# Performance work log

Hardware: AMD Instinct MI355X
Metric: run time of the kernel (lower is better)

## Reference

```python
import jax, jax.numpy as jnp
import numpy as np

N = 50000      # nodes
E = 600000     # edges (before self loops)
F_IN = 128     # num_features
HID = 64       # num_hidden (per-head out channels of conv1)
HEADS = 8
NCLS = 16      # num_classes
NC = 16        # n_components (k_ricci feature dim)
NCP = 16       # n_components_p (e_poinc feature dim)


def _glorot(key, shape):
    lim = float(np.sqrt(6.0 / (shape[0] + shape[1])))
    return jax.random.uniform(key, shape, jnp.float32, -lim, lim)


def setup_inputs() -> dict:
    key = jax.random.key(0)
    ks = jax.random.split(key, 16)
    H1 = HEADS * HID  # 512
    return {
        "x": jax.random.normal(ks[0], (N, F_IN), jnp.float32),
        "edge_index": jax.random.randint(ks[1], (2, E), 0, N, jnp.int32),
        "alpha": jnp.ones((), jnp.float32),  # alpha_hp scalar
        "k_ricci": jax.random.normal(ks[2], (E + N, NC), jnp.float32),
        "e_poinc": jax.random.normal(ks[3], (N, NCP), jnp.float32),
        # conv1 params
        "W_src1": _glorot(ks[4], (F_IN, H1)),
        "h1_w1": _glorot(ks[5], (NC, HID)),
        "h1_w2": _glorot(ks[6], (HID, HID)),
        "h1_b2": jnp.zeros((HID,), jnp.float32),
        "p1_w1": _glorot(ks[7], (NCP, H1)),
        "p1_w2": _glorot(ks[8], (H1, H1)),
        "p1_b2": jnp.zeros((H1,), jnp.float32),
        "bias1": jnp.zeros((H1,), jnp.float32),
        # conv2 params (heads=1, concat=False)
        "W_src2": _glorot(ks[9], (H1, NCLS)),
        "h2_w1": _glorot(ks[10], (NC, NCLS)),
        "h2_w2": _glorot(ks[11], (NCLS, NCLS)),
        "h2_b2": jnp.zeros((NCLS,), jnp.float32),
        "p2_w1": _glorot(ks[12], (NCP, NCLS)),
        "p2_w2": _glorot(ks[13], (NCLS, NCLS)),
        "p2_b2": jnp.zeros((NCLS,), jnp.float32),
        "bias2": jnp.zeros((NCLS,), jnp.float32),
    }


def _segment_softmax(logits, seg, n):
    # PyG-style softmax over variable-sized segments, per channel.
    m = jax.ops.segment_max(logits, seg, num_segments=n)
    e = jnp.exp(logits - m[seg])
    s = jax.ops.segment_sum(e, seg, num_segments=n)
    return e / (s[seg] + 1e-16)


def _gat_layer(x, src, dst, k_ricci, e_poinc, alpha_hp,
               W_src, hw1, hw2, hb2, pw1, pw2, pb2, bias, H, C, concat):
    n = x.shape[0]
    xh = (x @ W_src).reshape(n, H, C)                                   # [N,H,C]
    # hmpnn MLP on per-edge Ricci features, then segment-softmax over SOURCE node
    edge_w = jax.nn.leaky_relu(k_ricci @ hw1, 0.2) @ hw2 + hb2          # [E',C]
    a = _segment_softmax(edge_w, src, n)                                # [E',C]
    msg = a[:, None, :] * xh[src]                                       # [E',H,C]
    agg = jax.ops.segment_sum(msg, dst, num_segments=n)                 # [N,H,C]
    out = agg.reshape(n, H * C) if concat else agg.mean(axis=1)
    out = out + bias
    # ham MLP on per-node Poincare features (+ extra leaky_relu, slope 0.01)
    p = jax.nn.leaky_relu(jax.nn.leaky_relu(e_poinc @ pw1, 0.2) @ pw2 + pb2, 0.01)
    return out + alpha_hp * p


def reference(x, edge_index, alpha, k_ricci, e_poinc,
              W_src1, h1_w1, h1_w2, h1_b2, p1_w1, p1_w2, p1_b2, bias1,
              W_src2, h2_w1, h2_w2, h2_b2, p2_w1, p2_w2, p2_b2, bias2):
    n = x.shape[0]
    loops = jnp.arange(n, dtype=edge_index.dtype)
    src = jnp.concatenate([edge_index[0], loops])   # add_self_loops
    dst = jnp.concatenate([edge_index[1], loops])
    h = _gat_layer(x, src, dst, k_ricci, e_poinc, alpha,
                   W_src1, h1_w1, h1_w2, h1_b2, p1_w1, p1_w2, p1_b2, bias1,
                   HEADS, HID, True)
    h = jax.nn.relu(h)
    o = _gat_layer(h, src, dst, k_ricci, e_poinc, alpha,
                   W_src2, h2_w1, h2_w2, h2_b2, p2_w1, p2_w2, p2_b2, bias2,
                   1, NCLS, False)
    return jax.nn.log_softmax(o, axis=1)
```

## Files before the change

kernel.cpp:

```cpp
#include <hip/hip_runtime.h>
#include <math.h>

#define N_NODES 50000
#define M_PAD   50048
#define N_EDGES 600000
#define E_TOT   650000
#define F_IN    128
#define HID     64
#define HEADS   8
#define H1      512
#define NCLS    16
#define NC      16
#define NCP     16
#define NBLK    ((N_NODES + 255) / 256)

typedef unsigned short u16;
typedef unsigned char  u8;
typedef __attribute__((ext_vector_type(8))) short short8;
typedef __attribute__((ext_vector_type(4))) float f32x4;
typedef __attribute__((ext_vector_type(2))) float f32x2;

__device__ __forceinline__ float bf2f(u16 h) {
    return __uint_as_float(((unsigned)h) << 16);
}
__device__ __forceinline__ u16 f2bf(float f) {
    unsigned u = __float_as_uint(f);
    u += 0x7fffu + ((u >> 16) & 1u);
    return (u16)(u >> 16);
}
__device__ __forceinline__ int edge_src(const int* __restrict__ ei, int e) {
    return (e < N_EDGES) ? ei[e] : (e - N_EDGES);
}
__device__ __forceinline__ int edge_dst(const int* __restrict__ ei, int e) {
    return (e < N_EDGES) ? ei[N_EDGES + e] : (e - N_EDGES);
}

__global__ __launch_bounds__(256) void count_k(const int* __restrict__ ei,
                                               int* __restrict__ src_cnt, int* __restrict__ dst_cnt) {
    int e = blockIdx.x * 256 + threadIdx.x;
    if (e >= E_TOT) return;
    atomicAdd(&src_cnt[edge_src(ei, e)], 1);
    atomicAdd(&dst_cnt[edge_dst(ei, e)], 1);
}

__global__ __launch_bounds__(256) void scanA_k(const int* __restrict__ src_cnt,
                                               const int* __restrict__ dst_cnt,
                                               int* __restrict__ partials) {
    int pass = blockIdx.x >= NBLK;
    int b = blockIdx.x - pass * NBLK;
    const int* cnt = pass ? dst_cnt : src_cnt;
    int idx = b * 256 + threadIdx.x;
    int v = (idx < N_NODES) ? cnt[idx] : 0;
    __shared__ int red[4];
    #pragma unroll
    for (int off = 32; off; off >>= 1) v += __shfl_down(v, off, 64);
    if ((threadIdx.x & 63) == 0) red[threadIdx.x >> 6] = v;
    __syncthreads();
    if (threadIdx.x == 0) partials[blockIdx.x] = red[0] + red[1] + red[2] + red[3];
}

__global__ __launch_bounds__(512) void scanB_k(int* __restrict__ partials) {
    __shared__ int lds[512];
    int t = threadIdx.x;
    int seg = t >> 8, i = t & 255;
    int v = (i < NBLK) ? partials[seg * NBLK + i] : 0;
    lds[t] = v;
    __syncthreads();
    for (int d = 1; d < 256; d <<= 1) {
        int x = (i >= d) ? lds[seg * 256 + i - d] : 0;
        __syncthreads();
        lds[t] += x;
        __syncthreads();
    }
    if (i < NBLK) partials[seg * NBLK + i] = lds[t] - v;
}

__global__ __launch_bounds__(256) void scanC_k(const int* __restrict__ src_cnt,
                                               const int* __restrict__ dst_cnt,
                                               const int* __restrict__ partials,
                                               int* __restrict__ src_off, int* __restrict__ dst_off) {
    int pass = blockIdx.x >= NBLK;
    int b = blockIdx.x - pass * NBLK;
    const int* cnt = pass ? dst_cnt : src_cnt;
    int* off = pass ? dst_off : src_off;
    int base = partials[blockIdx.x];
    __shared__ int lds[256];
    int t = threadIdx.x;
    int idx = b * 256 + t;
    int v = (idx < N_NODES) ? cnt[idx] : 0;
    lds[t] = v;
    __syncthreads();
    for (int d = 1; d < 256; d <<= 1) {
        int x = (t >= d) ? lds[t - d] : 0;
        __syncthreads();
        lds[t] += x;
        __syncthreads();
    }
    if (idx < N_NODES) off[idx] = base + lds[t] - v;
    if (b == 0 && t == 0) off[N_NODES] = E_TOT;
}

__global__ __launch_bounds__(256) void fill_csr_k(const int* __restrict__ ei,
                                                  const int* __restrict__ src_off, const int* __restrict__ dst_off,
                                                  int* __restrict__ src_cur, int* __restrict__ dst_cur,
                                                  int* __restrict__ src_list, int* __restrict__ rkd,
                                                  int* __restrict__ dsrc) {
    int e = blockIdx.x * 256 + threadIdx.x;
    if (e >= E_TOT) return;
    int s = edge_src(ei, e), d = edge_dst(ei, e);
    int pd = atomicAdd(&dst_cur[d], 1);
    int rd = dst_off[d] + pd;
    rkd[e] = rd;
    dsrc[rd] = s;
    int ps = atomicAdd(&src_cur[s], 1);
    src_list[src_off[s] + ps] = rd;
}

__global__ __launch_bounds__(256) void conv_a_k(const float* __restrict__ A, u16* __restrict__ Ap,
                                                int M, int Mp, int K) {
    int i = blockIdx.x * 256 + threadIdx.x;
    int total = (K >> 3) * Mp;
    if (i >= total) return;
    int r = i % Mp;
    int kb = i / Mp;
    u16* o = Ap + (size_t)i * 8;
    u16 tmp[8];
    if (r < M) {
        const float* a = A + (size_t)r * K + kb * 8;
        #pragma unroll
        for (int j = 0; j < 8; ++j) tmp[j] = f2bf(a[j]);
    } else {
        #pragma unroll
        for (int j = 0; j < 8; ++j) tmp[j] = 0;
    }
    *(ushort4*)o = *(ushort4*)tmp;
    *(ushort4*)(o + 4) = *(ushort4*)(tmp + 4);
}

__global__ __launch_bounds__(256) void conv_b_k(const float* __restrict__ B, u16* __restrict__ Bp,
                                                int K, int N) {
    int i = blockIdx.x * 256 + threadIdx.x;
    int total = (K >> 3) * N;
    if (i >= total) return;
    int n = i % N;
    int kb = i / N;
    u16 tmp[8];
    #pragma unroll
    for (int j = 0; j < 8; ++j) tmp[j] = f2bf(B[(size_t)(kb * 8 + j) * N + n]);
    u16* o = Bp + (size_t)i * 8;
    *(ushort4*)o = *(ushort4*)tmp;
    *(ushort4*)(o + 4) = *(ushort4*)(tmp + 4);
}

__device__ __forceinline__ void wfrag_one(const float* W, u16* o, int i, int K, int N) {
    int j = i & 7, lane = (i >> 3) & 63, rest = i >> 9;
    int nt = rest % (N / 16), ks = rest / (N / 16);
    int lm = lane & 15, quad = lane >> 4;
    int k = ks * 32 + quad * 8 + j, n = nt * 16 + lm;
    o[i] = (k < K) ? f2bf(W[(size_t)k * N + n]) : (u16)0;
}
__global__ __launch_bounds__(256) void wfrag_all_k(
    const float* __restrict__ h1w1, const float* __restrict__ h1w2,
    const float* __restrict__ h2w1, const float* __restrict__ h2w2,
    u16* __restrict__ w1f, u16* __restrict__ w2f,
    u16* __restrict__ w3f, u16* __restrict__ w4f) {
    int i = blockIdx.x * 256 + threadIdx.x;
    if (i < 2048)      wfrag_one(h1w1, w1f, i, 16, 64);
    else if (i < 6144) wfrag_one(h1w2, w2f, i - 2048, 64, 64);
    else if (i < 6656) wfrag_one(h2w1, w3f, i - 6144, 16, 16);
    else if (i < 7168) wfrag_one(h2w2, w4f, i - 6656, 16, 16);
}

template<int EPI>
__global__ __launch_bounds__(256) void mfma_gemm_k(
    const u16* __restrict__ Ap, const u16* __restrict__ Bp, u16* __restrict__ C,
    int M, int Mp, int Nn, int K,
    const float* __restrict__ bias, const u16* __restrict__ extra,
    const float* __restrict__ bias2, const float* __restrict__ alpha_p)
{
    const int t = threadIdx.x;
    const int wave = t >> 6, lane = t & 63;
    const int wm = (wave >> 1) * 64, wn = (wave & 1) * 64;
    const int bm = blockIdx.y * 128, bn = blockIdx.x * 128;
    const int lm = lane & 15, quad = lane >> 4;

    size_t rbase[4], cbase[4];
    #pragma unroll
    for (int mi = 0; mi < 4; ++mi) rbase[mi] = (size_t)(bm + wm + mi * 16 + lm) * 8;
    #pragma unroll
    for (int nj = 0; nj < 4; ++nj) cbase[nj] = (size_t)(bn + wn + nj * 16 + lm) * 8;

    f32x4 acc[4][4] = {};

    for (int k0 = 0; k0 < K; k0 += 32) {
        int kb = (k0 >> 3) + quad;
        size_t abase = (size_t)kb * Mp * 8;
        size_t bbase = (size_t)kb * Nn * 8;
        short8 af[4], bf_[4];
        #pragma unroll
        for (int mi = 0; mi < 4; ++mi) af[mi] = *(const short8*)(Ap + abase + rbase[mi]);
        #pragma unroll
        for (int nj = 0; nj < 4; ++nj) bf_[nj] = *(const short8*)(Bp + bbase + cbase[nj]);
        #pragma unroll
        for (int mi = 0; mi < 4; ++mi)
            #pragma unroll
            for (int nj = 0; nj < 4; ++nj)
                acc[mi][nj] = __builtin_amdgcn_mfma_f32_16x16x32_bf16(af[mi], bf_[nj], acc[mi][nj], 0, 0, 0);
    }

    const int orow = bm + wm + quad * 4;
    const int ocol = bn + wn + lm;
    if (EPI == 0) {
        #pragma unroll
        for (int mi = 0; mi < 4; ++mi)
            #pragma unroll
            for (int r = 0; r < 4; ++r) {
                int rr = orow + mi * 16 + r;
                if (rr >= M) continue;
                #pragma unroll
                for (int nj = 0; nj < 4; ++nj)
                    C[(size_t)rr * Nn + ocol + nj * 16] = f2bf(acc[mi][nj][r]);
            }
    } else {
        float alpha = *alpha_p;
        #pragma unroll
        for (int mi = 0; mi < 4; ++mi)
            #pragma unroll
            for (int r = 0; r < 4; ++r) {
                int rr = orow + mi * 16 + r;
                if (rr >= M) continue;
                #pragma unroll
                for (int nj = 0; nj < 4; ++nj) {
                    int c = ocol + nj * 16;
                    float v = acc[mi][nj][r] + bias[c];
                    v = v > 0.f ? v : 0.01f * v;
                    float o = bf2f(extra[(size_t)rr * Nn + c]) + bias2[c] + alpha * v;
                    o = fmaxf(o, 0.f);
                    C[(size_t)rr * Nn + c] = f2bf(o);
                }
            }
    }
}

__global__ __launch_bounds__(256) void gemm_t1_k(
    const float* __restrict__ ep, const float* __restrict__ W, u16* __restrict__ t1p)
{
    __shared__ float Bs[16][64];
    const int bm = blockIdx.y * 64, bn = blockIdx.x * 64;
    const int t = threadIdx.x;
    const int tx = t & 15, ty = t >> 4;
    *(float4*)&Bs[t >> 4][(t & 15) * 4] = *(const float4*)&W[(size_t)(t >> 4) * H1 + bn + (t & 15) * 4];
    __syncthreads();
    const int r0 = bm + ty * 4;
    const int c0 = bn + tx * 4;
    for (int i = 0; i < 4; ++i) {
        int r = r0 + i;
        if (r >= N_NODES) continue;
        float av[16];
        #pragma unroll
        for (int j4 = 0; j4 < 16; j4 += 4) {
            float4 v = *(const float4*)(ep + (size_t)r * NCP + j4);
            av[j4] = v.x; av[j4 + 1] = v.y; av[j4 + 2] = v.z; av[j4 + 3] = v.w;
        }
        u16 pk[4];
        #pragma unroll
        for (int q = 0; q < 4; ++q) {
            float s = 0.f;
            #pragma unroll
            for (int k = 0; k < 16; ++k) s = fmaf(av[k], Bs[k][tx * 4 + q], s);
            s = s > 0.f ? s : 0.2f * s;
            pk[q] = f2bf(s);
        }
        u16* o = t1p + ((size_t)(c0 >> 3) * M_PAD + r) * 8 + (c0 & 7);
        *(ushort4*)o = *(ushort4*)pk;
    }
}

__global__ __launch_bounds__(256) void gemm_n16_k(
    const u16* __restrict__ A, const float* __restrict__ B, float* __restrict__ C,
    int M, int K)
{
    __shared__ float As[16][64];
    __shared__ float Bs[64][16];
    const int row0 = blockIdx.x * 16;
    const int t = threadIdx.x;
    const int r = t >> 4, c = t & 15;
    const int ar = t >> 4, ak4 = (t & 15) * 4;
    const int bk = t >> 2, bc4 = (t & 3) * 4;
    float acc = 0.f;
    for (int k0 = 0; k0 < K; k0 += 64) {
        float4 av = make_float4(0.f, 0.f, 0.f, 0.f);
        if (row0 + ar < M) {
            ushort4 h4 = *(const ushort4*)(A + (size_t)(row0 + ar) * K + k0 + ak4);
            av = make_float4(bf2f(h4.x), bf2f(h4.y), bf2f(h4.z), bf2f(h4.w));
        }
        *(float4*)&As[ar][ak4] = av;
        *(float4*)&Bs[bk][bc4] = *(const float4*)(B + (size_t)(k0 + bk) * 16 + bc4);
        __syncthreads();
        #pragma unroll
        for (int kk = 0; kk < 64; ++kk)
            acc = fmaf(As[r][kk], Bs[kk][c], acc);
        __syncthreads();
    }
    if (row0 + r < M) C[(size_t)(row0 + r) * 16 + c] = acc;
}

#define TSTR 72
__global__ __launch_bounds__(256) void edge_mlps_k(
    const float* __restrict__ kr, const int* __restrict__ rkd,
    const u16* __restrict__ w1f, const u16* __restrict__ w2f, const float* __restrict__ b2a,
    const u16* __restrict__ w3f, const u16* __restrict__ w4f, const float* __restrict__ b2b,
    u16* __restrict__ ebd, u16* __restrict__ ebd2)
{
    __shared__ __align__(16) u16 T[4][16 * TSTR];
    const int t = threadIdx.x, wv = t >> 6, lane = t & 63;
    const int lm = lane & 15, quad = lane >> 4;
    const int tile = blockIdx.x * 4 + wv;
    const int e0 = tile * 16;
    if (e0 >= E_TOT) return;
    u16* Tw = T[wv];

    short8 W1[4], W2[2][4];
    #pragma unroll
    for (int nt = 0; nt < 4; ++nt) W1[nt] = *(const short8*)(w1f + ((size_t)nt * 64 + lane) * 8);
    #pragma unroll
    for (int ks = 0; ks < 2; ++ks)
        #pragma unroll
        for (int nt = 0; nt < 4; ++nt)
            W2[ks][nt] = *(const short8*)(w2f + (((size_t)ks * 4 + nt) * 64 + lane) * 8);
    short8 W3 = *(const short8*)(w3f + (size_t)lane * 8);
    short8 W4 = *(const short8*)(w4f + (size_t)lane * 8);
    float b2av[4];
    #pragma unroll
    for (int nt = 0; nt < 4; ++nt) b2av[nt] = b2a[nt * 16 + lm];
    float b2bv = b2b[lm];

    short8 af = {};
    if (quad < 2) {
        const float* kp = kr + (size_t)(e0 + lm) * NC + quad * 8;
        float4 v0 = *(const float4*)kp;
        float4 v1 = *(const float4*)(kp + 4);
        u16 tmp[8] = {f2bf(v0.x), f2bf(v0.y), f2bf(v0.z), f2bf(v0.w),
                      f2bf(v1.x), f2bf(v1.y), f2bf(v1.z), f2bf(v1.w)};
        af = *(const short8*)tmp;
    }

    f32x4 a1[4] = {};
    #pragma unroll
    for (int nt = 0; nt < 4; ++nt)
        a1[nt] = __builtin_amdgcn_mfma_f32_16x16x32_bf16(af, W1[nt], a1[nt], 0, 0, 0);
    #pragma unroll
    for (int nt = 0; nt < 4; ++nt)
        #pragma unroll
        for (int r = 0; r < 4; ++r) {
            float v = a1[nt][r];
            v = v > 0.f ? v : 0.2f * v;
            Tw[(quad * 4 + r) * TSTR + nt * 16 + lm] = f2bf(v);
        }
    __builtin_amdgcn_s_waitcnt(0);

    short8 a2[2];
    #pragma unroll
    for (int ks = 0; ks < 2; ++ks)
        a2[ks] = *(const short8*)&Tw[lm * TSTR + ks * 32 + quad * 8];
    f32x4 c2[4] = {};
    #pragma unroll
    for (int nt = 0; nt < 4; ++nt)
        #pragma unroll
        for (int ks = 0; ks < 2; ++ks)
            c2[nt] = __builtin_amdgcn_mfma_f32_16x16x32_bf16(a2[ks], W2[ks][nt], c2[nt], 0, 0, 0);
    #pragma unroll
    for (int nt = 0; nt < 4; ++nt)
        #pragma unroll
        for (int r = 0; r < 4; ++r)
            Tw[(quad * 4 + r) * TSTR + nt * 16 + lm] = f2bf(__expf(c2[nt][r] + b2av[nt]));
    __builtin_amdgcn_s_waitcnt(0);
    #pragma unroll
    for (int p = 0; p < 2; ++p) {
        int c = p * 64 + lane;
        int row = c >> 3, off = (c & 7) * 8;
        int rd = rkd[e0 + row];
        short8 v = *(const short8*)&Tw[row * TSTR + off];
        *(short8*)(ebd + (size_t)rd * HID + off) = v;
    }

    f32x4 b1 = __builtin_amdgcn_mfma_f32_16x16x32_bf16(af, W3, (f32x4){}, 0, 0, 0);
    __builtin_amdgcn_s_waitcnt(0);
    #pragma unroll
    for (int r = 0; r < 4; ++r) {
        float v = b1[r];
        v = v > 0.f ? v : 0.2f * v;
        Tw[(quad * 4 + r) * TSTR + lm] = f2bf(v);
    }
    __builtin_amdgcn_s_waitcnt(0);
    short8 a3 = *(const short8*)&Tw[lm * TSTR + quad * 8];
    f32x4 c3 = __builtin_amdgcn_mfma_f32_16x16x32_bf16(a3, W4, (f32x4){}, 0, 0, 0);
    #pragma unroll
    for (int r = 0; r < 4; ++r)
        Tw[(quad * 4 + r) * TSTR + lm] = f2bf(__expf(c3[r] + b2bv));
    __builtin_amdgcn_s_waitcnt(0);
    if (lane < 32) {
        int row = lane >> 1, off = (lane & 1) * 8;
        int rd = rkd[e0 + row];
        short8 v = *(const short8*)&Tw[row * TSTR + off];
        *(short8*)(ebd2 + (size_t)rd * NCLS + off) = v;
    }
}

__global__ __launch_bounds__(256) void s1inv_k(
    const u16* __restrict__ ebd, const int* __restrict__ src_off, const int* __restrict__ src_list,
    u16* __restrict__ xb)
{
    __shared__ float sinv[4][64];
    int gid = blockIdx.x * 256 + threadIdx.x;
    int wid = gid >> 6, lane = gid & 63, wv = threadIdx.x >> 6;
    if (wid >= N_NODES) return;
    int o0 = src_off[wid], o1 = src_off[wid + 1];
    float s0 = 0.f, s1 = 0.f, s2 = 0.f, s3 = 0.f;
    int i = o0;
    for (; i + 3 < o1; i += 4) {
        int l0 = src_list[i], l1 = src_list[i + 1], l2 = src_list[i + 2], l3 = src_list[i + 3];
        s0 += bf2f(ebd[(size_t)l0 * HID + lane]);
        s1 += bf2f(ebd[(size_t)l1 * HID + lane]);
        s2 += bf2f(ebd[(size_t)l2 * HID + lane]);
        s3 += bf2f(ebd[(size_t)l3 * HID + lane]);
    }
    for (; i < o1; ++i) {
        int sl = src_list[i];
        s0 += bf2f(ebd[(size_t)sl * HID + lane]);
    }
    sinv[wv][lane] = 1.f / (((s0 + s1) + (s2 + s3)) + 1e-16f);
    __builtin_amdgcn_s_waitcnt(0);

    const u16* xr = xb + (size_t)wid * H1 + lane * 8;
    short8 x8 = *(const short8*)xr;
    float y[8];
    #pragma unroll
    for (int j = 0; j < 8; ++j)
        y[j] = bf2f((u16)x8[j]) * sinv[wv][(lane * 8 + j) & 63];
    int p0 = 0, p1 = 0;
    p0 = __builtin_amdgcn_cvt_pk_fp8_f32(y[0], y[1], p0, false);
    p0 = __builtin_amdgcn_cvt_pk_fp8_f32(y[2], y[3], p0, true);
    p1 = __builtin_amdgcn_cvt_pk_fp8_f32(y[4], y[5], p1, false);
    p1 = __builtin_amdgcn_cvt_pk_fp8_f32(y[6], y[7], p1, true);
    uint2 pk; pk.x = (unsigned)p0; pk.y = (unsigned)p1;
    *(uint2*)((u8*)xb + (size_t)wid * (H1 * 2) + lane * 8) = pk;
}

__global__ __launch_bounds__(256) void msg1_k(
    const u16* __restrict__ ebd, const u8* __restrict__ xq,
    const int* __restrict__ dsrc, const int* __restrict__ dst_off,
    u16* __restrict__ aggb)
{
    int gid = blockIdx.x * 256 + threadIdx.x;
    int wid = gid >> 6, lane = gid & 63;
    if (wid >= N_NODES) return;
    int o0 = dst_off[wid], o1 = dst_off[wid + 1];
    const int a_off = (lane & 7) * 8;
    float acc[8] = {};
    int i = o0;
    for (; i + 3 < o1; i += 4) {
        int s0 = __builtin_nontemporal_load(dsrc + i);
        int s1 = __builtin_nontemporal_load(dsrc + i + 1);
        int s2 = __builtin_nontemporal_load(dsrc + i + 2);
        int s3 = __builtin_nontemporal_load(dsrc + i + 3);
        short8 a0 = __builtin_nontemporal_load((const short8*)(ebd + (size_t)i * HID + a_off));
        short8 a1 = __builtin_nontemporal_load((const short8*)(ebd + (size_t)(i + 1) * HID + a_off));
        short8 a2 = __builtin_nontemporal_load((const short8*)(ebd + (size_t)(i + 2) * HID + a_off));
        short8 a3 = __builtin_nontemporal_load((const short8*)(ebd + (size_t)(i + 3) * HID + a_off));
        uint2 q0 = *(const uint2*)(xq + (size_t)s0 * 1024 + lane * 8);
        uint2 q1 = *(const uint2*)(xq + (size_t)s1 * 1024 + lane * 8);
        uint2 q2 = *(const uint2*)(xq + (size_t)s2 * 1024 + lane * 8);
        uint2 q3 = *(const uint2*)(xq + (size_t)s3 * 1024 + lane * 8);
        const uint2 qs[4] = {q0, q1, q2, q3};
        const short8 as[4] = {a0, a1, a2, a3};
        #pragma unroll
        for (int u = 0; u < 4; ++u) {
            f32x2 d0 = __builtin_amdgcn_cvt_pk_f32_fp8((int)qs[u].x, false);
            f32x2 d1 = __builtin_amdgcn_cvt_pk_f32_fp8((int)qs[u].x, true);
            f32x2 d2 = __builtin_amdgcn_cvt_pk_f32_fp8((int)qs[u].y, false);
            f32x2 d3 = __builtin_amdgcn_cvt_pk_f32_fp8((int)qs[u].y, true);
            float xv[8] = {d0.x, d0.y, d1.x, d1.y, d2.x, d2.y, d3.x, d3.y};
            #pragma unroll
            for (int j = 0; j < 8; ++j)
                acc[j] = fmaf(bf2f((u16)as[u][j]), xv[j], acc[j]);
        }
    }
    for (; i < o1; ++i) {
        int s = __builtin_nontemporal_load(dsrc + i);
        short8 a8 = __builtin_nontemporal_load((const short8*)(ebd + (size_t)i * HID + a_off));
        uint2 q = *(const uint2*)(xq + (size_t)s * 1024 + lane * 8);
        f32x2 d0 = __builtin_amdgcn_cvt_pk_f32_fp8((int)q.x, false);
        f32x2 d1 = __builtin_amdgcn_cvt_pk_f32_fp8((int)q.x, true);
        f32x2 d2 = __builtin_amdgcn_cvt_pk_f32_fp8((int)q.y, false);
        f32x2 d3 = __builtin_amdgcn_cvt_pk_f32_fp8((int)q.y, true);
        float xv[8] = {d0.x, d0.y, d1.x, d1.y, d2.x, d2.y, d3.x, d3.y};
        #pragma unroll
        for (int j = 0; j < 8; ++j)
            acc[j] = fmaf(bf2f((u16)a8[j]), xv[j], acc[j]);
    }
    u16 pk[8];
    #pragma unroll
    for (int j = 0; j < 8; ++j) pk[j] = f2bf(acc[j]);
    __builtin_nontemporal_store(*(const short8*)pk, (short8*)(aggb + (size_t)wid * H1 + lane * 8));
}

__global__ __launch_bounds__(256) void s2sum_k(
    const u16* __restrict__ ebd2, const int* __restrict__ src_off, const int* __restrict__ src_list,
    float* __restrict__ inv2)
{
    int t = threadIdx.x;
    int g = blockIdx.x * 16 + (t >> 4), c = t & 15;
    if (g >= N_NODES) return;
    int o0 = src_off[g], o1 = src_off[g + 1];
    float sum = 0.f;
    for (int i = o0; i < o1; ++i) {
        int sl = src_list[i];
        sum += bf2f(ebd2[(size_t)sl * NCLS + c]);
    }
    inv2[(size_t)g * NCLS + c] = 1.f / (sum + 1e-16f);
}

__global__ __launch_bounds__(256) void msg2_k(
    const u16* __restrict__ ebd2, const float* __restrict__ inv2,
    const float* __restrict__ xh2, const int* __restrict__ dsrc,
    const int* __restrict__ dst_off, float* __restrict__ agg2)
{
    int t = threadIdx.x;
    int g = blockIdx.x * 16 + (t >> 4), c = t & 15;
    if (g >= N_NODES) return;
    int o0 = dst_off[g], o1 = dst_off[g + 1];
    float acc = 0.f;
    for (int i = o0; i < o1; ++i) {
        int s = dsrc[i];
        float a = bf2f(ebd2[(size_t)i * NCLS + c]) * inv2[(size_t)s * NCLS + c];
        acc = fmaf(a, xh2[(size_t)s * NCLS + c], acc);
    }
    agg2[(size_t)g * NCLS + c] = acc;
}

__global__ __launch_bounds__(256) void final_k(
    const float* __restrict__ agg2, const float* __restrict__ ep,
    const float* __restrict__ pw1, const float* __restrict__ pw2,
    const float* __restrict__ pb2, const float* __restrict__ bias,
    const float* __restrict__ alpha_p, float* __restrict__ out)
{
    __shared__ float s1w[256], s2w[256], sb[16], sbias[16];
    const int t = threadIdx.x;
    s1w[t] = pw1[t];
    s2w[t] = pw2[t];
    if (t < 16) { sb[t] = pb2[t]; sbias[t] = bias[t]; }
    __syncthreads();
    const int v = blockIdx.x * 256 + t;
    if (v >= N_NODES) return;
    float alpha = *alpha_p;
    float e_[16];
    #pragma unroll
    for (int j4 = 0; j4 < 16; j4 += 4) {
        float4 vv = *(const float4*)(ep + (size_t)v * 16 + j4);
        e_[j4] = vv.x; e_[j4 + 1] = vv.y; e_[j4 + 2] = vv.z; e_[j4 + 3] = vv.w;
    }
    float t2[16];
    #pragma unroll
    for (int c = 0; c < 16; ++c) {
        float s = 0.f;
        #pragma unroll
        for (int j = 0; j < 16; ++j) s = fmaf(e_[j], s1w[j * 16 + c], s);
        t2[c] = s > 0.f ? s : 0.2f * s;
    }
    float o[16];
    #pragma unroll
    for (int c4 = 0; c4 < 16; c4 += 4) {
        float4 ag = *(const float4*)(agg2 + (size_t)v * 16 + c4);
        float agv[4] = {ag.x, ag.y, ag.z, ag.w};
        #pragma unroll
        for (int q = 0; q < 4; ++q) {
            int c = c4 + q;
            float p = sb[c];
            #pragma unroll
            for (int j = 0; j < 16; ++j) p = fmaf(t2[j], s2w[j * 16 + c], p);
            p = p > 0.f ? p : 0.01f * p;
            o[c] = agv[q] + sbias[c] + alpha * p;
        }
    }
    float mx = o[0];
    #pragma unroll
    for (int c = 1; c < 16; ++c) mx = fmaxf(mx, o[c]);
    float se = 0.f;
    #pragma unroll
    for (int c = 0; c < 16; ++c) se += expf(o[c] - mx);
    float lse = mx + logf(se);
    #pragma unroll
    for (int c4 = 0; c4 < 16; c4 += 4)
        *(float4*)(out + (size_t)v * 16 + c4) =
            make_float4(o[c4] - lse, o[c4 + 1] - lse, o[c4 + 2] - lse, o[c4 + 3] - lse);
}

extern "C" void kernel_launch(void* const* d_in, const int* in_sizes, int n_in,
                              void* d_out, int out_size, void* d_ws, size_t ws_size,
                              hipStream_t stream) {
    const float* x    = (const float*)d_in[0];
    const int*   ei   = (const int*)d_in[1];
    const float* alpha= (const float*)d_in[2];
    const float* kr   = (const float*)d_in[3];
    const float* ep   = (const float*)d_in[4];
    const float* W1   = (const float*)d_in[5];
    const float* h1w1 = (const float*)d_in[6];
    const float* h1w2 = (const float*)d_in[7];
    const float* h1b2 = (const float*)d_in[8];
    const float* p1w1 = (const float*)d_in[9];
    const float* p1w2 = (const float*)d_in[10];
    const float* p1b2 = (const float*)d_in[11];
    const float* b1   = (const float*)d_in[12];
    const float* W2   = (const float*)d_in[13];
    const float* h2w1 = (const float*)d_in[14];
    const float* h2w2 = (const float*)d_in[15];
    const float* h2b2 = (const float*)d_in[16];
    const float* p2w1 = (const float*)d_in[17];
    const float* p2w2 = (const float*)d_in[18];
    const float* p2b2 = (const float*)d_in[19];
    const float* b2   = (const float*)d_in[20];
    float* out = (float*)d_out;

    char* p = (char*)d_ws;
    auto alloc = [&](size_t bytes) { char* r = p; p += (bytes + 255) & ~(size_t)255; return r; };

    char* r0    = alloc((size_t)64 * M_PAD * 16);
    u16*  xb    = (u16*)r0;
    u16*  t1p   = (u16*)r0;
    u16*  aggb  = (u16*)alloc((size_t)N_NODES * H1 * 2);
    char* ebr   = alloc((size_t)E_TOT * HID * 2);
    u16*  ebd   = (u16*)ebr;
    u16*  hb    = (u16*)ebr;
    u16*  ebd2  = (u16*)alloc((size_t)E_TOT * NCLS * 2);
    u16*  xp    = (u16*)alloc((size_t)16 * M_PAD * 16);
    u16*  W1p   = (u16*)alloc((size_t)16 * H1 * 16);
    u16*  p1w2p = (u16*)alloc((size_t)64 * H1 * 16);
    u16*  w1f   = (u16*)alloc(2048 * 2);
    u16*  w2f   = (u16*)alloc(4096 * 2);
    u16*  w3f   = (u16*)alloc(512 * 2);
    u16*  w4f   = (u16*)alloc(512 * 2);
    int* src_cnt  = (int*)alloc(N_NODES * 4);
    int* dst_cnt  = (int*)alloc(N_NODES * 4);
    int* src_cur  = (int*)alloc(N_NODES * 4);
    int* dst_cur  = (int*)alloc(N_NODES * 4);
    int* partials = (int*)alloc(2 * NBLK * 4);
    int* src_off  = (int*)alloc((N_NODES + 1) * 4);
    int* dst_off  = (int*)alloc((N_NODES + 1) * 4);
    int* src_list = (int*)alloc((size_t)E_TOT * 4);
    int* rkd      = (int*)alloc((size_t)E_TOT * 4);
    int* dsrc     = (int*)alloc((size_t)E_TOT * 4);
    float* xh2  = (float*)alloc((size_t)N_NODES * NCLS * 4);
    float* agg2 = (float*)alloc((size_t)N_NODES * NCLS * 4);
    float* inv2 = (float*)alloc((size_t)N_NODES * NCLS * 4);

    const dim3 blk(256);
    const int EB = (E_TOT + 255) / 256;
    const int WB = (N_NODES * 64 + 255) / 256;
    const int GB16 = (N_NODES + 15) / 16;
    const dim3 gmm(512 / 128, M_PAD / 128);
    const int MLPB = (E_TOT / 16 + 3) / 4;

    hipMemsetAsync(src_cnt, 0, (char*)partials - (char*)src_cnt, stream);
    count_k<<<EB, blk, 0, stream>>>(ei, src_cnt, dst_cnt);
    scanA_k<<<2 * NBLK, blk, 0, stream>>>(src_cnt, dst_cnt, partials);
    scanB_k<<<1, 512, 0, stream>>>(partials);
    scanC_k<<<2 * NBLK, blk, 0, stream>>>(src_cnt, dst_cnt, partials, src_off, dst_off);
    fill_csr_k<<<EB, blk, 0, stream>>>(ei, src_off, dst_off, src_cur, dst_cur, src_list, rkd, dsrc);
    conv_a_k<<<(16 * M_PAD + 255) / 256, blk, 0, stream>>>(x, xp, N_NODES, M_PAD, F_IN);
    conv_b_k<<<(16 * H1 + 255) / 256, blk, 0, stream>>>(W1, W1p, F_IN, H1);
    conv_b_k<<<(64 * H1 + 255) / 256, blk, 0, stream>>>(p1w2, p1w2p, H1, H1);
    wfrag_all_k<<<28, blk, 0, stream>>>(h1w1, h1w2, h2w1, h2w2, w1f, w2f, w3f, w4f);

    mfma_gemm_k<0><<<gmm, blk, 0, stream>>>(xp, W1p, xb, N_NODES, M_PAD, H1, F_IN,
                                            nullptr, nullptr, nullptr, nullptr);
    edge_mlps_k<<<MLPB, blk, 0, stream>>>(kr, rkd, w1f, w2f, h1b2, w3f, w4f, h2b2, ebd, ebd2);
    s1inv_k<<<WB, blk, 0, stream>>>(ebd, src_off, src_list, xb);
    msg1_k<<<WB, blk, 0, stream>>>(ebd, (const u8*)xb, dsrc, dst_off, aggb);
    gemm_t1_k<<<dim3(8, (N_NODES + 63) / 64), blk, 0, stream>>>(ep, p1w1, t1p);
    mfma_gemm_k<3><<<gmm, blk, 0, stream>>>(t1p, p1w2p, hb, N_NODES, M_PAD, H1, H1,
                                            p1b2, aggb, b1, alpha);

    gemm_n16_k<<<(N_NODES + 15) / 16, blk, 0, stream>>>(hb, W2, xh2, N_NODES, H1);
    s2sum_k<<<GB16, blk, 0, stream>>>(ebd2, src_off, src_list, inv2);
    msg2_k<<<GB16, blk, 0, stream>>>(ebd2, inv2, xh2, dsrc, dst_off, agg2);
    final_k<<<(N_NODES + 255) / 256, blk, 0, stream>>>(agg2, ep, p2w1, p2w2, p2b2, b2, alpha, out);
}
```

Measured before the change: 683.4 us.

## Double-buffer MFMA GEMM tiles via direct global-to-LDS loads, XCD-aware block remap

The bf16 MFMA GEMM now stages A and B k-slices into LDS with global_load_lds in a double-buffered loop, overlapping the next tile's fetch with the current MFMA work. Blocks are remapped so consecutive tiles land on the same XCD for better L2 reuse. The epilogue transposes accumulators through swizzled LDS so each thread writes 32 contiguous bf16 outputs with 16-byte stores and reads the extra input vectorised. The price is extra LDS traffic and barriers, and the hardcoded 4-column grid assumption ties the remap to N=512.

Result: no change. 688.0 us (+0.7%).

```diff
diff --git a/kernel.cpp b/kernel.cpp
--- a/kernel.cpp
+++ b/kernel.cpp
@@ -33,6 +33,12 @@
 }
 __device__ __forceinline__ int edge_dst(const int* __restrict__ ei, int e) {
     return (e < N_EDGES) ? ei[N_EDGES + e] : (e - N_EDGES);
+}
+
+__device__ __forceinline__ void gload16(const void* g, void* l) {
+    __builtin_amdgcn_global_load_lds(
+        (const __attribute__((address_space(1))) unsigned int*)g,
+        (__attribute__((address_space(3))) unsigned int*)l, 16, 0, 0);
 }
 
 __global__ __launch_bounds__(256) void count_k(const int* __restrict__ ei,
@@ -178,67 +184,120 @@
     const float* __restrict__ bias, const u16* __restrict__ extra,
     const float* __restrict__ bias2, const float* __restrict__ alpha_p)
 {
+    __shared__ __align__(16) u16 LB[4][4096];
     const int t = threadIdx.x;
     const int wave = t >> 6, lane = t & 63;
     const int wm = (wave >> 1) * 64, wn = (wave & 1) * 64;
-    const int bm = blockIdx.y * 128, bn = blockIdx.x * 128;
     const int lm = lane & 15, quad = lane >> 4;
 
-    size_t rbase[4], cbase[4];
-    #pragma unroll
-    for (int mi = 0; mi < 4; ++mi) rbase[mi] = (size_t)(bm + wm + mi * 16 + lm) * 8;
-    #pragma unroll
-    for (int nj = 0; nj < 4; ++nj) cbase[nj] = (size_t)(bn + wn + nj * 16 + lm) * 8;
+    const int nwg = (int)(gridDim.y << 2);
+    const int bid = (int)(blockIdx.y * 4 + blockIdx.x);
+    const int qq = nwg >> 3, rr8 = nwg & 7;
+    const int xcd = bid & 7, idx = bid >> 3;
+    const int wg = (xcd < rr8 ? xcd * (qq + 1) : rr8 * (qq + 1) + (xcd - rr8) * qq) + idx;
+    const int bn = (wg & 3) * 128;
+    const int bm = (wg >> 2) * 128;
+
+    const char* Ab = (const char*)Ap;
+    const char* Bb = (const char*)Bp;
 
     f32x4 acc[4][4] = {};
-
-    for (int k0 = 0; k0 < K; k0 += 32) {
-        int kb = (k0 >> 3) + quad;
-        size_t abase = (size_t)kb * Mp * 8;
-        size_t bbase = (size_t)kb * Nn * 8;
-        short8 af[4], bf_[4];
-        #pragma unroll
-        for (int mi = 0; mi < 4; ++mi) af[mi] = *(const short8*)(Ap + abase + rbase[mi]);
-        #pragma unroll
-        for (int nj = 0; nj < 4; ++nj) bf_[nj] = *(const short8*)(Bp + bbase + cbase[nj]);
+    const int NT = K >> 5;
+
+    auto stage = [&](int buf, int ts) {
+        const int kb0 = ts * 4;
+        #pragma unroll
+        for (int h = 0; h < 2; ++h) {
+            const int ob = h * 4096 + wave * 1024;
+            const int kb = kb0 + (ob >> 11);
+            const int rem = (ob & 1024) + lane * 16;
+            gload16(Ab + ((size_t)kb * Mp + bm) * 16 + rem, (char*)LB[buf] + ob);
+            gload16(Bb + ((size_t)kb * Nn + bn) * 16 + rem, (char*)LB[2 + buf] + ob);
+        }
+    };
+    auto compute = [&](int cb) {
+        const u16* As = LB[cb];
+        const u16* Bs = LB[2 + cb];
+        short8 af[4], bfv[4];
+        #pragma unroll
+        for (int mi = 0; mi < 4; ++mi)
+            af[mi] = *(const short8*)(As + quad * 1024 + (wm + mi * 16 + lm) * 8);
+        #pragma unroll
+        for (int nj = 0; nj < 4; ++nj)
+            bfv[nj] = *(const short8*)(Bs + quad * 1024 + (wn + nj * 16 + lm) * 8);
         #pragma unroll
         for (int mi = 0; mi < 4; ++mi)
             #pragma unroll
             for (int nj = 0; nj < 4; ++nj)
-                acc[mi][nj] = __builtin_amdgcn_mfma_f32_16x16x32_bf16(af[mi], bf_[nj], acc[mi][nj], 0, 0, 0);
-    }
-
-    const int orow = bm + wm + quad * 4;
-    const int ocol = bn + wn + lm;
-    if (EPI == 0) {
-        #pragma unroll
-        for (int mi = 0; mi < 4; ++mi)
+                acc[mi][nj] = __builtin_amdgcn_mfma_f32_16x16x32_bf16(af[mi], bfv[nj], acc[mi][nj], 0, 0, 0);
+    };
+
+    stage(0, 0);
+    __syncthreads();
+    int cur = 0;
+    for (int ts = 0; ts < NT - 1; ++ts) {
+        stage(cur ^ 1, ts + 1);
+        compute(cur);
+        __syncthreads();
+        cur ^= 1;
+    }
+    compute(cur);
+    __syncthreads();
+
+    float* Tf = (float*)LB;
+    const int lrow = t & 63, chunk = t >> 6;
+    const int col0 = chunk * 32;
+    const float alpha = (EPI == 0) ? 0.f : *alpha_p;
+    #pragma unroll
+    for (int pass = 0; pass < 2; ++pass) {
+        if ((wave >> 1) == pass) {
             #pragma unroll
-            for (int r = 0; r < 4; ++r) {
-                int rr = orow + mi * 16 + r;
-                if (rr >= M) continue;
+            for (int mi = 0; mi < 4; ++mi)
                 #pragma unroll
-                for (int nj = 0; nj < 4; ++nj)
-                    C[(size_t)rr * Nn + ocol + nj * 16] = f2bf(acc[mi][nj][r]);
+                for (int r4 = 0; r4 < 4; ++r4) {
+                    const int lr = mi * 16 + quad * 4 + r4;
+                    const int sw = (lr & 7) << 2;
+                    #pragma unroll
+                    for (int nj = 0; nj < 4; ++nj)
+                        Tf[lr * 128 + ((wn + nj * 16 + lm) ^ sw)] = acc[mi][nj][r4];
+                }
+        }
+        __syncthreads();
+        const int rr = bm + pass * 64 + lrow;
+        if (rr < M) {
+            const int sw = (lrow & 7) << 2;
+            float v[32];
+            #pragma unroll
+            for (int j4 = 0; j4 < 8; ++j4) {
+                float4 f = *(const float4*)&Tf[lrow * 128 + ((col0 + j4 * 4) ^ sw)];
+                v[j4 * 4] = f.x; v[j4 * 4 + 1] = f.y; v[j4 * 4 + 2] = f.z; v[j4 * 4 + 3] = f.w;
             }
-    } else {
-        float alpha = *alpha_p;
-        #pragma unroll
-        for (int mi = 0; mi < 4; ++mi)
-            #pragma unroll
-            for (int r = 0; r < 4; ++r) {
-                int rr = orow + mi * 16 + r;
-                if (rr >= M) continue;
+            const int gc0 = bn + col0;
+            u16 pk[32];
+            if (EPI == 0) {
                 #pragma unroll
-                for (int nj = 0; nj < 4; ++nj) {
-                    int c = ocol + nj * 16;
-                    float v = acc[mi][nj][r] + bias[c];
-                    v = v > 0.f ? v : 0.01f * v;
-                    float o = bf2f(extra[(size_t)rr * Nn + c]) + bias2[c] + alpha * v;
-                    o = fmaxf(o, 0.f);
-                    C[(size_t)rr * Nn + c] = f2bf(o);
+                for (int j = 0; j < 32; ++j) pk[j] = f2bf(v[j]);
+            } else {
+                const u16* ex = extra + (size_t)rr * Nn + gc0;
+                #pragma unroll
+                for (int g = 0; g < 4; ++g) {
+                    short8 e8 = *(const short8*)(ex + g * 8);
+                    #pragma unroll
+                    for (int j = 0; j < 8; ++j) {
+                        const int cj = g * 8 + j;
+                        float vv = v[cj] + bias[gc0 + cj];
+                        vv = vv > 0.f ? vv : 0.01f * vv;
+                        float o = bf2f((u16)e8[j]) + bias2[gc0 + cj] + alpha * vv;
+                        o = fmaxf(o, 0.f);
+                        pk[cj] = f2bf(o);
+                    }
                 }
             }
+            #pragma unroll
+            for (int g = 0; g < 4; ++g)
+                *(short8*)(C + (size_t)rr * Nn + gc0 + g * 8) = *(const short8*)&pk[g * 8];
+        }
+        __syncthreads();
     }
 }
 
```
